# Optimization experiments

Measured on AMD Instinct MI355X. Metric: run time of the kernel, lower is better.

## Reference

```python
import jax, jax.numpy as jnp
import numpy as np

N_NODES = 100_000
N_EDGES = 1_600_000
IN_DIM = 500
HID = 128
OUT = 16
DEG = 3          # Chebyshev 'order' -> DEG+1 basis terms
N_KAN_USED = 2   # forward applies kan_layers[:num_layers-1] with num_layers=3


def spmm(edge_index, h):
    # torch.sparse.mm(A, h) with A = COO(edge_index, ones, (N, N)):
    # out[row] = sum over edges of h[col]
    return jax.ops.segment_sum(h[edge_index[1]], edge_index[0], num_segments=N_NODES)


def cheb_kan(h, coeffs):
    # ChebyKANLayer: t = tanh(h); basis T_k(t) = cos(k*arccos(t)) computed via
    # the (mathematically identical, numerically stable) recurrence.
    t = jnp.tanh(h)                                  # [N, HID]
    Ts = [jnp.ones_like(t), t]
    for _ in range(DEG - 1):
        Ts.append(2.0 * t * Ts[-1] - Ts[-2])
    basis = jnp.stack(Ts, axis=-1)                   # [N, HID, DEG+1]
    return jnp.einsum('nid,iod->no', basis, coeffs)  # [N, HID]


def setup_inputs() -> dict:
    key = jax.random.key(0)
    ks = jax.random.split(key, 6)
    x = jax.random.normal(ks[0], (N_NODES, IN_DIM), dtype=jnp.float32)
    edge_index = jax.random.randint(ks[1], (2, N_EDGES), 0, N_NODES)
    W_in = jax.random.normal(ks[2], (IN_DIM, HID), dtype=jnp.float32) / np.sqrt(IN_DIM)
    cheb_coeffs = jax.random.normal(ks[3], (N_KAN_USED, HID, HID, DEG + 1),
                                    dtype=jnp.float32) / (HID * (DEG + 1))
    W_out = jax.random.normal(ks[4], (HID, OUT), dtype=jnp.float32) / np.sqrt(HID)
    return {"x": x, "edge_index": edge_index, "W_in": W_in,
            "cheb_coeffs": cheb_coeffs, "W_out": W_out}


def reference(x, edge_index, W_in, cheb_coeffs, W_out):
    h = x @ W_in                      # linear_input (no bias)
    # dropout is identity at inference
    h = spmm(edge_index, h)           # sparse adjacency aggregation
    for l in range(N_KAN_USED):
        h = cheb_kan(h, cheb_coeffs[l])
        h = spmm(edge_index, h)
    logits = h @ W_out                # output_layer (no bias)
    return jax.nn.log_softmax(logits, axis=-1)
```

## Files before the change

### kernel.cpp

```cpp
#include <hip/hip_runtime.h>
#include <hip/hip_bf16.h>

#define N_NODES 100000
#define N_EDGES 1600000
#define IN_DIM  500
#define HID     128
#define KDIM    512
#define NB      782
#define BCAP    4096

typedef __attribute__((ext_vector_type(8))) short bf16x8;
typedef __attribute__((ext_vector_type(4))) float f32x4;

__device__ inline short f2bf(float x) {
    union { float f; unsigned u; } v; v.f = x;
    unsigned r = (v.u + 0x7FFFu + ((v.u >> 16) & 1u)) >> 16;
    return (short)r;
}
__device__ inline float bf_lo(unsigned u) { union { unsigned u; float f; } v; v.u = u << 16; return v.f; }
__device__ inline float bf_hi(unsigned u) { union { unsigned u; float f; } v; v.u = u & 0xFFFF0000u; return v.f; }
__device__ inline float bf2f(unsigned short s) { union { unsigned u; float f; } v; v.u = ((unsigned)s) << 16; return v.f; }


__global__ __launch_bounds__(256) void bin_kernel(const int* __restrict__ ei,
                                                  int* __restrict__ bcnt,
                                                  unsigned* __restrict__ buf) {
    int e = blockIdx.x * 256 + threadIdx.x;
    if (e < N_EDGES) {
        int r = ei[e];
        int c = ei[N_EDGES + e];
        int b = r >> 7;
        int p = atomicAdd(&bcnt[b * 16], 1);
        if (p < BCAP) buf[b * BCAP + p] = ((unsigned)(r & 127) << 17) | (unsigned)c;
    }
}

__global__ __launch_bounds__(1024) void bscan_kernel(const int* __restrict__ bcnt,
                                                     int* __restrict__ bbase) {
    __shared__ int buf[1024];
    const int tid = threadIdx.x;
    int v = (tid < NB) ? bcnt[tid * 16] : 0;
    buf[tid] = v;
    __syncthreads();
    for (int off = 1; off < 1024; off <<= 1) {
        int t = (tid >= off) ? buf[tid - off] : 0;
        __syncthreads();
        buf[tid] += t;
        __syncthreads();
    }
    if (tid < NB) bbase[tid] = buf[tid] - v;
}

__global__ __launch_bounds__(256) void place_kernel(const unsigned* __restrict__ buf,
                                                    const int* __restrict__ bcnt,
                                                    const int* __restrict__ bbase,
                                                    int* __restrict__ row_start,
                                                    int* __restrict__ col_sorted) {
    __shared__ int hist[128];
    __shared__ int scan[128];
    __shared__ int cur[128];
    const int b = blockIdx.x, tid = threadIdx.x;
    int cnt = bcnt[b * 16]; if (cnt > BCAP) cnt = BCAP;
    const int base = bbase[b];
    if (tid < 128) hist[tid] = 0;
    __syncthreads();
    for (int i = tid; i < cnt; i += 256)
        atomicAdd(&hist[buf[b * BCAP + i] >> 17], 1);
    __syncthreads();
    if (tid < 128) scan[tid] = hist[tid];
    __syncthreads();
    for (int off = 1; off < 128; off <<= 1) {
        int t = (tid < 128 && tid >= off) ? scan[tid - off] : 0;
        __syncthreads();
        if (tid < 128) scan[tid] += t;
        __syncthreads();
    }
    if (tid < 128) {
        int excl = scan[tid] - hist[tid] + base;
        cur[tid] = excl;
        int r = b * 128 + tid;
        if (r < N_NODES) row_start[r] = excl;
        if (r == N_NODES - 1) row_start[N_NODES] = excl + hist[tid];
    }
    __syncthreads();
    for (int i = tid; i < cnt; i += 256) {
        unsigned u = buf[b * BCAP + i];
        int rl = (int)(u >> 17);
        int c  = (int)(u & 0x1FFFFu);
        int pos = atomicAdd(&cur[rl], 1);
        col_sorted[pos] = c;
    }
}

__global__ __launch_bounds__(256) void repack_cheb(const float* __restrict__ cheb,
                                                   unsigned short* __restrict__ Bmat) {
    int idx = blockIdx.x * 256 + threadIdx.x;
    int l = idx >> 16;
    int rem = idx & 65535;
    int o = rem >> 9;
    int k = rem & 511;
    int i = k >> 2;
    int d = k & 3;
    Bmat[idx] = (unsigned short)f2bf(cheb[l * 65536 + i * 512 + o * 4 + d]);
}
__global__ __launch_bounds__(256) void repack_w(const float* __restrict__ W,
                                                unsigned short* __restrict__ Wmat) {
    int idx = blockIdx.x * 256 + threadIdx.x;
    int o = idx >> 9;
    int k = idx & 511;
    Wmat[idx] = (k < IN_DIM) ? (unsigned short)f2bf(W[k * HID + o]) : 0;
}

__global__ __launch_bounds__(256, 3) void gemm_xw(const float* __restrict__ x,
                                                  const unsigned short* __restrict__ Wmat,
                                                  unsigned short* __restrict__ out) {
    __shared__ __align__(16) short As[2][128][40];
    __shared__ __align__(16) short Bs[2][128][40];
    const int tid  = threadIdx.x;
    const int lane = tid & 63;
    const int wave = tid >> 6;
    const int quad = lane >> 4;
    const int l16  = lane & 15;
    const int n0   = blockIdx.x * 128;
    const int lr   = tid >> 1;
    const int lh   = tid & 1;
    const int bm   = tid >> 2;
    const int bkq  = tid & 3;

    int nA = n0 + lr; if (nA >= N_NODES) nA = N_NODES - 1;
    const float* __restrict__ xrow = x + (long)nA * IN_DIM;

    f32x4 acc[2][8];
#pragma unroll
    for (int mt = 0; mt < 2; mt++)
#pragma unroll
        for (int nt = 0; nt < 8; nt++)
#pragma unroll
            for (int r = 0; r < 4; r++) acc[mt][nt][r] = 0.f;

    auto loadA = [&](int kt, float (&v)[16]) {
        const int kb = kt * 32 + lh * 16;
        if (kb + 16 <= IN_DIM) {
            const float4* s4 = (const float4*)(xrow + kb);
            float4 a0 = s4[0], a1 = s4[1], a2 = s4[2], a3 = s4[3];
            v[0]=a0.x; v[1]=a0.y; v[2]=a0.z; v[3]=a0.w;
            v[4]=a1.x; v[5]=a1.y; v[6]=a1.z; v[7]=a1.w;
            v[8]=a2.x; v[9]=a2.y; v[10]=a2.z; v[11]=a2.w;
            v[12]=a3.x; v[13]=a3.y; v[14]=a3.z; v[15]=a3.w;
        } else {
#pragma unroll
            for (int q = 0; q < 16; q++) v[q] = (kb + q < IN_DIM) ? xrow[kb + q] : 0.f;
        }
    };
    auto loadB = [&](int kt, bf16x8 (&w)[2]) {
        w[0] = *(const bf16x8*)&Wmat[bm * 512 + kt * 32 + bkq * 8];
        w[1] = *(const bf16x8*)&Wmat[(bm + 64) * 512 + kt * 32 + bkq * 8];
    };
    auto storeA = [&](int buf, const float (&v)[16]) {
        short t[16];
#pragma unroll
        for (int q = 0; q < 16; q++) t[q] = f2bf(v[q]);
        *(bf16x8*)&As[buf][lr][lh * 16]     = *(bf16x8*)&t[0];
        *(bf16x8*)&As[buf][lr][lh * 16 + 8] = *(bf16x8*)&t[8];
    };
    auto storeB = [&](int buf, const bf16x8 (&w)[2]) {
        *(bf16x8*)&Bs[buf][bm][bkq * 8]      = w[0];
        *(bf16x8*)&Bs[buf][bm + 64][bkq * 8] = w[1];
    };
    auto mfmaTile = [&](int buf) {
        bf16x8 a0 = *(const bf16x8*)&As[buf][wave * 32 + l16][quad * 8];
        bf16x8 a1 = *(const bf16x8*)&As[buf][wave * 32 + 16 + l16][quad * 8];
#pragma unroll
        for (int nt = 0; nt < 8; nt++) {
            bf16x8 b = *(const bf16x8*)&Bs[buf][nt * 16 + l16][quad * 8];
            acc[0][nt] = __builtin_amdgcn_mfma_f32_16x16x32_bf16(a0, b, acc[0][nt], 0, 0, 0);
            acc[1][nt] = __builtin_amdgcn_mfma_f32_16x16x32_bf16(a1, b, acc[1][nt], 0, 0, 0);
        }
    };

    float  va[16], vb[16];
    bf16x8 wa[2],  wb[2];
    loadA(0, va); loadB(0, wa);
    for (int kt = 0; kt < 16; kt += 2) {
        storeA(0, va); storeB(0, wa);
        loadA(kt + 1, vb); loadB(kt + 1, wb);
        __syncthreads();
        mfmaTile(0);
        storeA(1, vb); storeB(1, wb);
        if (kt + 2 < 16) { loadA(kt + 2, va); loadB(kt + 2, wa); }
        __syncthreads();
        mfmaTile(1);
    }

#pragma unroll
    for (int mt = 0; mt < 2; mt++) {
        int mrow = n0 + wave * 32 + mt * 16 + quad * 4;
#pragma unroll
        for (int r = 0; r < 4; r++) {
            int n = mrow + r;
            if (n < N_NODES) {
#pragma unroll
                for (int nt = 0; nt < 8; nt++)
                    out[(long)n * HID + nt * 16 + l16] = (unsigned short)f2bf(acc[mt][nt][r]);
            }
        }
    }
}

__global__ __launch_bounds__(256, 3) void cheb_gemm(const unsigned short* __restrict__ h,
                                                    const unsigned short* __restrict__ Bmat,
                                                    unsigned short* __restrict__ out) {
    __shared__ __align__(16) short As[2][128][40];
    __shared__ __align__(16) short Bs[2][128][40];
    const int tid  = threadIdx.x;
    const int lane = tid & 63;
    const int wave = tid >> 6;
    const int quad = lane >> 4;
    const int l16  = lane & 15;
    const int n0   = blockIdx.x * 128;
    const int lr   = tid >> 1;
    const int lh   = tid & 1;
    const int bm   = tid >> 2;
    const int bkq  = tid & 3;

    int nA = n0 + lr; if (nA >= N_NODES) nA = N_NODES - 1;
    const unsigned short* __restrict__ hrow = h + (long)nA * HID;

    f32x4 acc[2][8];
#pragma unroll
    for (int mt = 0; mt < 2; mt++)
#pragma unroll
        for (int nt = 0; nt < 8; nt++)
#pragma unroll
            for (int r = 0; r < 4; r++) acc[mt][nt][r] = 0.f;

    auto loadA = [&](int kt, ushort4& v) {
        v = *(const ushort4*)(hrow + kt * 8 + lh * 4);
    };
    auto loadB = [&](int kt, bf16x8 (&w)[2]) {
        w[0] = *(const bf16x8*)&Bmat[bm * 512 + kt * 32 + bkq * 8];
        w[1] = *(const bf16x8*)&Bmat[(bm + 64) * 512 + kt * 32 + bkq * 8];
    };
    auto storeA = [&](int buf, const ushort4& v) {
        float hx[4] = {bf2f(v.x), bf2f(v.y), bf2f(v.z), bf2f(v.w)};
        short t[16];
#pragma unroll
        for (int q = 0; q < 4; q++) {
            float xx = fminf(fmaxf(hx[q], -15.f), 15.f);
            float e  = __expf(2.f * xx);
            float tt = (e - 1.f) / (e + 1.f);
            float T2 = 2.f * tt * tt - 1.f;
            float T3 = 2.f * tt * T2 - tt;
            t[q * 4 + 0] = (short)0x3F80;
            t[q * 4 + 1] = f2bf(tt);
            t[q * 4 + 2] = f2bf(T2);
            t[q * 4 + 3] = f2bf(T3);
        }
        *(bf16x8*)&As[buf][lr][lh * 16]     = *(bf16x8*)&t[0];
        *(bf16x8*)&As[buf][lr][lh * 16 + 8] = *(bf16x8*)&t[8];
    };
    auto storeB = [&](int buf, const bf16x8 (&w)[2]) {
        *(bf16x8*)&Bs[buf][bm][bkq * 8]      = w[0];
        *(bf16x8*)&Bs[buf][bm + 64][bkq * 8] = w[1];
    };
    auto mfmaTile = [&](int buf) {
        bf16x8 a0 = *(const bf16x8*)&As[buf][wave * 32 + l16][quad * 8];
        bf16x8 a1 = *(const bf16x8*)&As[buf][wave * 32 + 16 + l16][quad * 8];
#pragma unroll
        for (int nt = 0; nt < 8; nt++) {
            bf16x8 b = *(const bf16x8*)&Bs[buf][nt * 16 + l16][quad * 8];
            acc[0][nt] = __builtin_amdgcn_mfma_f32_16x16x32_bf16(a0, b, acc[0][nt], 0, 0, 0);
            acc[1][nt] = __builtin_amdgcn_mfma_f32_16x16x32_bf16(a1, b, acc[1][nt], 0, 0, 0);
        }
    };

    ushort4 va, vb;
    bf16x8  wa[2], wb[2];
    loadA(0, va); loadB(0, wa);
    for (int kt = 0; kt < 16; kt += 2) {
        storeA(0, va); storeB(0, wa);
        loadA(kt + 1, vb); loadB(kt + 1, wb);
        __syncthreads();
        mfmaTile(0);
        storeA(1, vb); storeB(1, wb);
        if (kt + 2 < 16) { loadA(kt + 2, va); loadB(kt + 2, wa); }
        __syncthreads();
        mfmaTile(1);
    }

#pragma unroll
    for (int mt = 0; mt < 2; mt++) {
        int mrow = n0 + wave * 32 + mt * 16 + quad * 4;
#pragma unroll
        for (int r = 0; r < 4; r++) {
            int n = mrow + r;
            if (n < N_NODES) {
#pragma unroll
                for (int nt = 0; nt < 8; nt++)
                    out[(long)n * HID + nt * 16 + l16] = (unsigned short)f2bf(acc[mt][nt][r]);
            }
        }
    }
}

__global__ __launch_bounds__(256) void spmm_gather(const int* __restrict__ row_start,
                                                   const int* __restrict__ col_sorted,
                                                   const unsigned short* __restrict__ h,
                                                   unsigned short* __restrict__ out) {
    const int wid  = (blockIdx.x * 256 + threadIdx.x) >> 6;
    const int lane = threadIdx.x & 63;
    const int sub  = lane >> 4;
    const int fl   = lane & 15;
    if (wid >= N_NODES) return;
    const int s = row_start[wid];
    const int e = row_start[wid + 1];
    const uint4* __restrict__ h4 = (const uint4*)h;

    float a[8], b[8];
#pragma unroll
    for (int q = 0; q < 8; q++) { a[q] = 0.f; b[q] = 0.f; }

    int j = s;
    for (; j + 8 <= e; j += 8) {
        int c0 = col_sorted[j + sub];
        int c1 = col_sorted[j + 4 + sub];
        uint4 u0 = h4[c0 * 16 + fl];
        uint4 u1 = h4[c1 * 16 + fl];
        a[0] += bf_lo(u0.x); a[1] += bf_hi(u0.x);
        a[2] += bf_lo(u0.y); a[3] += bf_hi(u0.y);
        a[4] += bf_lo(u0.z); a[5] += bf_hi(u0.z);
        a[6] += bf_lo(u0.w); a[7] += bf_hi(u0.w);
        b[0] += bf_lo(u1.x); b[1] += bf_hi(u1.x);
        b[2] += bf_lo(u1.y); b[3] += bf_hi(u1.y);
        b[4] += bf_lo(u1.z); b[5] += bf_hi(u1.z);
        b[6] += bf_lo(u1.w); b[7] += bf_hi(u1.w);
    }
    for (; j < e; j += 4) {
        int idx = j + sub;
        float m = (idx < e) ? 1.f : 0.f;
        int ci = (idx < e) ? idx : (e - 1);
        int c = col_sorted[ci];
        uint4 u = h4[c * 16 + fl];
        a[0] = fmaf(m, bf_lo(u.x), a[0]); a[1] = fmaf(m, bf_hi(u.x), a[1]);
        a[2] = fmaf(m, bf_lo(u.y), a[2]); a[3] = fmaf(m, bf_hi(u.y), a[3]);
        a[4] = fmaf(m, bf_lo(u.z), a[4]); a[5] = fmaf(m, bf_hi(u.z), a[5]);
        a[6] = fmaf(m, bf_lo(u.w), a[6]); a[7] = fmaf(m, bf_hi(u.w), a[7]);
    }
#pragma unroll
    for (int q = 0; q < 8; q++) a[q] += b[q];
#pragma unroll
    for (int q = 0; q < 8; q++) {
        a[q] += __shfl_xor(a[q], 16);
        a[q] += __shfl_xor(a[q], 32);
    }
    if (sub == 0) {
        unsigned w0 = (unsigned)(unsigned short)f2bf(a[0]) | ((unsigned)(unsigned short)f2bf(a[1]) << 16);
        unsigned w1 = (unsigned)(unsigned short)f2bf(a[2]) | ((unsigned)(unsigned short)f2bf(a[3]) << 16);
        unsigned w2 = (unsigned)(unsigned short)f2bf(a[4]) | ((unsigned)(unsigned short)f2bf(a[5]) << 16);
        unsigned w3 = (unsigned)(unsigned short)f2bf(a[6]) | ((unsigned)(unsigned short)f2bf(a[7]) << 16);
        uint4 pw; pw.x = w0; pw.y = w1; pw.z = w2; pw.w = w3;
        ((uint4*)out)[wid * 16 + fl] = pw;
    }
}

__global__ __launch_bounds__(256) void out_kernel(const unsigned short* __restrict__ h,
                                                  const float* __restrict__ Wo,
                                                  float* __restrict__ out) {
    __shared__ float Ws[HID * 16];
    __shared__ float Hs[16][HID];
    const int tid = threadIdx.x;
    const int n0 = blockIdx.x * 16;
    for (int idx = tid; idx < HID * 16; idx += 256) Ws[idx] = Wo[idx];
    const unsigned* h1 = (const unsigned*)h;
    for (int idx = tid; idx < 16 * 64; idx += 256) {
        int nl = idx >> 6;
        int kp = idx & 63;
        unsigned u = h1[(n0 + nl) * 64 + kp];
        Hs[nl][kp * 2]     = bf_lo(u);
        Hs[nl][kp * 2 + 1] = bf_hi(u);
    }
    __syncthreads();
    const int nl = tid >> 4;
    const int o  = tid & 15;
    float acc = 0.f;
#pragma unroll
    for (int k = 0; k < HID; k++) acc += Hs[nl][k] * Ws[k * 16 + o];
    float mx = acc;
#pragma unroll
    for (int m = 8; m >= 1; m >>= 1) mx = fmaxf(mx, __shfl_xor(mx, m));
    float ex = expf(acc - mx);
    float se = ex;
#pragma unroll
    for (int m = 8; m >= 1; m >>= 1) se += __shfl_xor(se, m);
    out[(n0 + nl) * 16 + o] = acc - mx - logf(se);
}


extern "C" void kernel_launch(void* const* d_in, const int* in_sizes, int n_in,
                              void* d_out, int out_size, void* d_ws, size_t ws_size,
                              hipStream_t stream) {
    const float* x     = (const float*)d_in[0];
    const int*   ei    = (const int*)d_in[1];
    const float* W_in  = (const float*)d_in[2];
    const float* cheb  = (const float*)d_in[3];
    const float* W_out = (const float*)d_in[4];
    float* out = (float*)d_out;

    char* p = (char*)d_ws;
    unsigned short* hA   = (unsigned short*)p; p += (size_t)N_NODES * HID * 2;
    unsigned short* hB   = (unsigned short*)p; p += (size_t)N_NODES * HID * 2;
    int*   col_sorted    = (int*)p;            p += (size_t)N_EDGES * 4;
    unsigned short* Bmat = (unsigned short*)p; p += (size_t)2 * HID * KDIM * 2;
    unsigned short* Wmat = (unsigned short*)p; p += (size_t)HID * KDIM * 2;
    int*   row_start     = (int*)p;            p += (size_t)(N_NODES + 1) * 4;
    int*   bcnt          = (int*)p;            p += (size_t)NB * 16 * 4;
    int*   bbase         = (int*)p;            p += (size_t)NB * 4;

    unsigned* bbuf = (unsigned*)hA;

    const int nblk_gemm = (N_NODES + 127) / 128;
    const int nblk_edge = N_EDGES / 256;
    const int nblk_spmm = (N_NODES + 3) / 4;
    const int nblk_out  = N_NODES / 16;

    hipMemsetAsync(bcnt, 0, (size_t)NB * 16 * 4, stream);
    bin_kernel<<<nblk_edge, 256, 0, stream>>>(ei, bcnt, bbuf);
    bscan_kernel<<<1, 1024, 0, stream>>>(bcnt, bbase);
    place_kernel<<<NB, 256, 0, stream>>>(bbuf, bcnt, bbase, row_start, col_sorted);
    repack_cheb<<<2 * HID * KDIM / 256, 256, 0, stream>>>(cheb, Bmat);
    repack_w<<<HID * KDIM / 256, 256, 0, stream>>>(W_in, Wmat);

    gemm_xw<<<nblk_gemm, 256, 0, stream>>>(x, Wmat, hA);
    spmm_gather<<<nblk_spmm, 256, 0, stream>>>(row_start, col_sorted, hA, hB);

    cheb_gemm<<<nblk_gemm, 256, 0, stream>>>(hB, Bmat, hA);
    spmm_gather<<<nblk_spmm, 256, 0, stream>>>(row_start, col_sorted, hA, hB);

    cheb_gemm<<<nblk_gemm, 256, 0, stream>>>(hB, Bmat + HID * KDIM, hA);
    spmm_gather<<<nblk_spmm, 256, 0, stream>>>(row_start, col_sorted, hA, hB);

    out_kernel<<<nblk_out, 256, 0, stream>>>(hB, W_out, out);
}
```

Before: 685.5 us.

## Fold output projection into last KAN layer and aggregate 16-wide logits

After: 650.2 us. -5.2%, faster.

```diff
diff --git a/kernel.cpp b/kernel.cpp
--- a/kernel.cpp
+++ b/kernel.cpp
@@ -95,13 +95,11 @@
 __global__ __launch_bounds__(256) void repack_cheb(const float* __restrict__ cheb,
                                                    unsigned short* __restrict__ Bmat) {
     int idx = blockIdx.x * 256 + threadIdx.x;
-    int l = idx >> 16;
-    int rem = idx & 65535;
-    int o = rem >> 9;
-    int k = rem & 511;
+    int o = idx >> 9;
+    int k = idx & 511;
     int i = k >> 2;
     int d = k & 3;
-    Bmat[idx] = (unsigned short)f2bf(cheb[l * 65536 + i * 512 + o * 4 + d]);
+    Bmat[idx] = (unsigned short)f2bf(cheb[i * 512 + o * 4 + d]);
 }
 __global__ __launch_bounds__(256) void repack_w(const float* __restrict__ W,
                                                 unsigned short* __restrict__ Wmat) {
@@ -109,6 +107,19 @@
     int o = idx >> 9;
     int k = idx & 511;
     Wmat[idx] = (k < IN_DIM) ? (unsigned short)f2bf(W[k * HID + o]) : 0;
+}
+__global__ __launch_bounds__(256) void repack_c2w(const float* __restrict__ cheb,
+                                                  const float* __restrict__ Wout,
+                                                  unsigned short* __restrict__ C2W) {
+    int idx = blockIdx.x * 256 + threadIdx.x;
+    if (idx >= 16 * 512) return;
+    int o16 = idx >> 9;
+    int k   = idx & 511;
+    const float* cb = cheb + 65536 + (k >> 2) * 512 + (k & 3);
+    float s = 0.f;
+#pragma unroll 4
+    for (int o = 0; o < 128; o++) s += cb[o * 4] * Wout[o * 16 + o16];
+    C2W[o16 * 512 + k] = (unsigned short)f2bf(s);
 }
 
 __global__ __launch_bounds__(256, 3) void gemm_xw(const float* __restrict__ x,
@@ -303,6 +314,91 @@
     }
 }
 
+__global__ __launch_bounds__(256, 3) void cheb16_gemm(const unsigned short* __restrict__ h,
+                                                      const unsigned short* __restrict__ C2W,
+                                                      float* __restrict__ z) {
+    __shared__ __align__(16) short As[2][128][40];
+    __shared__ __align__(16) short Bs16[16][520];
+    const int tid  = threadIdx.x;
+    const int lane = tid & 63;
+    const int wave = tid >> 6;
+    const int quad = lane >> 4;
+    const int l16  = lane & 15;
+    const int n0   = blockIdx.x * 128;
+    const int lr   = tid >> 1;
+    const int lh   = tid & 1;
+
+    {
+        int o16 = tid >> 4;
+        int seg = tid & 15;
+        *(bf16x8*)&Bs16[o16][seg * 32]      = *(const bf16x8*)&C2W[o16 * 512 + seg * 32];
+        *(bf16x8*)&Bs16[o16][seg * 32 + 8]  = *(const bf16x8*)&C2W[o16 * 512 + seg * 32 + 8];
+        *(bf16x8*)&Bs16[o16][seg * 32 + 16] = *(const bf16x8*)&C2W[o16 * 512 + seg * 32 + 16];
+        *(bf16x8*)&Bs16[o16][seg * 32 + 24] = *(const bf16x8*)&C2W[o16 * 512 + seg * 32 + 24];
+    }
+
+    int nA = n0 + lr; if (nA >= N_NODES) nA = N_NODES - 1;
+    const unsigned short* __restrict__ hrow = h + (long)nA * HID;
+
+    f32x4 acc[2];
+#pragma unroll
+    for (int mt = 0; mt < 2; mt++)
+#pragma unroll
+        for (int r = 0; r < 4; r++) acc[mt][r] = 0.f;
+
+    auto loadA = [&](int kt, ushort4& v) {
+        v = *(const ushort4*)(hrow + kt * 8 + lh * 4);
+    };
+    auto storeA = [&](int buf, const ushort4& v) {
+        float hx[4] = {bf2f(v.x), bf2f(v.y), bf2f(v.z), bf2f(v.w)};
+        short t[16];
+#pragma unroll
+        for (int q = 0; q < 4; q++) {
+            float xx = fminf(fmaxf(hx[q], -15.f), 15.f);
+            float e  = __expf(2.f * xx);
+            float tt = (e - 1.f) / (e + 1.f);
+            float T2 = 2.f * tt * tt - 1.f;
+            float T3 = 2.f * tt * T2 - tt;
+            t[q * 4 + 0] = (short)0x3F80;
+            t[q * 4 + 1] = f2bf(tt);
+            t[q * 4 + 2] = f2bf(T2);
+            t[q * 4 + 3] = f2bf(T3);
+        }
+        *(bf16x8*)&As[buf][lr][lh * 16]     = *(bf16x8*)&t[0];
+        *(bf16x8*)&As[buf][lr][lh * 16 + 8] = *(bf16x8*)&t[8];
+    };
+    auto mfmaTile = [&](int buf, int kt) {
+        bf16x8 a0 = *(const bf16x8*)&As[buf][wave * 32 + l16][quad * 8];
+        bf16x8 a1 = *(const bf16x8*)&As[buf][wave * 32 + 16 + l16][quad * 8];
+        bf16x8 b  = *(const bf16x8*)&Bs16[l16][kt * 32 + quad * 8];
+        acc[0] = __builtin_amdgcn_mfma_f32_16x16x32_bf16(a0, b, acc[0], 0, 0, 0);
+        acc[1] = __builtin_amdgcn_mfma_f32_16x16x32_bf16(a1, b, acc[1], 0, 0, 0);
+    };
+
+    ushort4 va, vb;
+    loadA(0, va);
+    for (int kt = 0; kt < 16; kt += 2) {
+        storeA(0, va);
+        loadA(kt + 1, vb);
+        __syncthreads();
+        mfmaTile(0, kt);
+        storeA(1, vb);
+        if (kt + 2 < 16) loadA(kt + 2, va);
+        __syncthreads();
+        mfmaTile(1, kt + 1);
+    }
+
+#pragma unroll
+    for (int mt = 0; mt < 2; mt++) {
+        int mrow = n0 + wave * 32 + mt * 16 + quad * 4;
+#pragma unroll
+        for (int r = 0; r < 4; r++) {
+            int n = mrow + r;
+            if (n < N_NODES) z[n * 16 + l16] = acc[mt][r];
+        }
+    }
+}
+
 __global__ __launch_bounds__(256) void spmm_gather(const int* __restrict__ row_start,
                                                    const int* __restrict__ col_sorted,
                                                    const unsigned short* __restrict__ h,
@@ -363,36 +459,43 @@
     }
 }
 
-__global__ __launch_bounds__(256) void out_kernel(const unsigned short* __restrict__ h,
-                                                  const float* __restrict__ Wo,
-                                                  float* __restrict__ out) {
-    __shared__ float Ws[HID * 16];
-    __shared__ float Hs[16][HID];
-    const int tid = threadIdx.x;
-    const int n0 = blockIdx.x * 16;
-    for (int idx = tid; idx < HID * 16; idx += 256) Ws[idx] = Wo[idx];
-    const unsigned* h1 = (const unsigned*)h;
-    for (int idx = tid; idx < 16 * 64; idx += 256) {
-        int nl = idx >> 6;
-        int kp = idx & 63;
-        unsigned u = h1[(n0 + nl) * 64 + kp];
-        Hs[nl][kp * 2]     = bf_lo(u);
-        Hs[nl][kp * 2 + 1] = bf_hi(u);
-    }
-    __syncthreads();
-    const int nl = tid >> 4;
-    const int o  = tid & 15;
-    float acc = 0.f;
-#pragma unroll
-    for (int k = 0; k < HID; k++) acc += Hs[nl][k] * Ws[k * 16 + o];
-    float mx = acc;
+__global__ __launch_bounds__(256) void spmm_out(const int* __restrict__ row_start,
+                                                const int* __restrict__ col_sorted,
+                                                const float* __restrict__ z,
+                                                float* __restrict__ out) {
+    const int wid  = (blockIdx.x * 256 + threadIdx.x) >> 6;
+    const int lane = threadIdx.x & 63;
+    const int sub  = lane >> 4;
+    const int fl   = lane & 15;
+    if (wid >= N_NODES) return;
+    const int s = row_start[wid];
+    const int e = row_start[wid + 1];
+
+    float a0 = 0.f, a1 = 0.f;
+    int j = s;
+    for (; j + 8 <= e; j += 8) {
+        int c0 = col_sorted[j + sub];
+        int c1 = col_sorted[j + 4 + sub];
+        a0 += z[c0 * 16 + fl];
+        a1 += z[c1 * 16 + fl];
+    }
+    for (; j < e; j += 4) {
+        int idx = j + sub;
+        float m = (idx < e) ? 1.f : 0.f;
+        int ci = (idx < e) ? idx : (e - 1);
+        a0 = fmaf(m, z[col_sorted[ci] * 16 + fl], a0);
+    }
+    float v = a0 + a1;
+    v += __shfl_xor(v, 16);
+    v += __shfl_xor(v, 32);
+    float mx = v;
 #pragma unroll
     for (int m = 8; m >= 1; m >>= 1) mx = fmaxf(mx, __shfl_xor(mx, m));
-    float ex = expf(acc - mx);
+    float ex = expf(v - mx);
     float se = ex;
 #pragma unroll
     for (int m = 8; m >= 1; m >>= 1) se += __shfl_xor(se, m);
-    out[(n0 + nl) * 16 + o] = acc - mx - logf(se);
+    if (sub == 0) out[wid * 16 + fl] = v - mx - logf(se);
 }
 
 
@@ -410,8 +513,10 @@
     unsigned short* hA   = (unsigned short*)p; p += (size_t)N_NODES * HID * 2;
     unsigned short* hB   = (unsigned short*)p; p += (size_t)N_NODES * HID * 2;
     int*   col_sorted    = (int*)p;            p += (size_t)N_EDGES * 4;
-    unsigned short* Bmat = (unsigned short*)p; p += (size_t)2 * HID * KDIM * 2;
+    unsigned short* Bmat = (unsigned short*)p; p += (size_t)HID * KDIM * 2;
     unsigned short* Wmat = (unsigned short*)p; p += (size_t)HID * KDIM * 2;
+    unsigned short* C2W  = (unsigned short*)p; p += (size_t)16 * KDIM * 2;
+    float* zbuf          = (float*)p;          p += (size_t)N_NODES * 16 * 4;
     int*   row_start     = (int*)p;            p += (size_t)(N_NODES + 1) * 4;
     int*   bcnt          = (int*)p;            p += (size_t)NB * 16 * 4;
     int*   bbase         = (int*)p;            p += (size_t)NB * 4;
@@ -421,14 +526,14 @@
     const int nblk_gemm = (N_NODES + 127) / 128;
     const int nblk_edge = N_EDGES / 256;
     const int nblk_spmm = (N_NODES + 3) / 4;
-    const int nblk_out  = N_NODES / 16;
 
     hipMemsetAsync(bcnt, 0, (size_t)NB * 16 * 4, stream);
     bin_kernel<<<nblk_edge, 256, 0, stream>>>(ei, bcnt, bbuf);
     bscan_kernel<<<1, 1024, 0, stream>>>(bcnt, bbase);
     place_kernel<<<NB, 256, 0, stream>>>(bbuf, bcnt, bbase, row_start, col_sorted);
-    repack_cheb<<<2 * HID * KDIM / 256, 256, 0, stream>>>(cheb, Bmat);
+    repack_cheb<<<HID * KDIM / 256, 256, 0, stream>>>(cheb, Bmat);
     repack_w<<<HID * KDIM / 256, 256, 0, stream>>>(W_in, Wmat);
+    repack_c2w<<<16 * KDIM / 256, 256, 0, stream>>>(cheb, W_out, C2W);
 
     gemm_xw<<<nblk_gemm, 256, 0, stream>>>(x, Wmat, hA);
     spmm_gather<<<nblk_spmm, 256, 0, stream>>>(row_start, col_sorted, hA, hB);
@@ -436,8 +541,6 @@
     cheb_gemm<<<nblk_gemm, 256, 0, stream>>>(hB, Bmat, hA);
     spmm_gather<<<nblk_spmm, 256, 0, stream>>>(row_start, col_sorted, hA, hB);
 
-    cheb_gemm<<<nblk_gemm, 256, 0, stream>>>(hB, Bmat + HID * KDIM, hA);
-    spmm_gather<<<nblk_spmm, 256, 0, stream>>>(row_start, col_sorted, hA, hB);
-
-    out_kernel<<<nblk_out, 256, 0, stream>>>(hB, W_out, out);
-}
+    cheb16_gemm<<<nblk_gemm, 256, 0, stream>>>(hB, C2W, zbuf);
+    spmm_out<<<nblk_spmm, 256, 0, stream>>>(row_start, col_sorted, zbuf, out);
+}
```
